# Kernel optimization log

Hardware: AMD Instinct MI355X
Metric: run time of the kernel (lower is better)

## Reference

```python
import jax, jax.numpy as jnp
import numpy as np

EMBED_DIM = 1024
NUM_HEADS = 16
SCALE = (EMBED_DIM // NUM_HEADS) ** -0.5  # 0.125


def setup_inputs() -> dict:
    key = jax.random.key(0)
    ks = jax.random.split(key, 9)
    B, S, E = 4, 2048, EMBED_DIM
    std = E ** -0.5
    x = jax.random.normal(ks[0], (B, S, E), dtype=jnp.float32)
    Wq = jax.random.normal(ks[1], (E, E), dtype=jnp.float32) * std
    bq = jax.random.normal(ks[2], (E,), dtype=jnp.float32) * 0.01
    Wk = jax.random.normal(ks[3], (E, E), dtype=jnp.float32) * std
    bk = jax.random.normal(ks[4], (E,), dtype=jnp.float32) * 0.01
    Wv = jax.random.normal(ks[5], (E, E), dtype=jnp.float32) * std
    bv = jax.random.normal(ks[6], (E,), dtype=jnp.float32) * 0.01
    Wo = jax.random.normal(ks[7], (E, E), dtype=jnp.float32) * std
    bo = jax.random.normal(ks[8], (E,), dtype=jnp.float32) * 0.01
    return {"x": x, "Wq": Wq, "bq": bq, "Wk": Wk, "bk": bk,
            "Wv": Wv, "bv": bv, "Wo": Wo, "bo": bo}


def reference(x, Wq, bq, Wk, bk, Wv, bv, Wo, bo):
    # torch nn.Linear: y = x @ W.T + b
    q = jnp.einsum('bse,fe->bsf', x, Wq) + bq   # [B,S,E]
    k = jnp.einsum('bse,fe->bsf', x, Wk) + bk
    v = jnp.einsum('bse,fe->bsf', x, Wv) + bv
    # Bilinear (no softmax) attention: scores = (Q K^T) * scale
    scores = jnp.einsum('bse,bte->bst', q, k) * SCALE  # [B,S,S]
    out = jnp.einsum('bst,bte->bse', scores, v)        # [B,S,E]
    return jnp.einsum('bse,fe->bsf', out, Wo) + bo
```

## Files before the change

### kernel.cpp

```cpp
#include <hip/hip_runtime.h>
#include <stdint.h>

typedef __bf16 bf16_t;
typedef __bf16 bf16x8 __attribute__((ext_vector_type(8)));
typedef __bf16 bf16x4 __attribute__((ext_vector_type(4)));
typedef float floatx4 __attribute__((ext_vector_type(4)));

__device__ __forceinline__ void async_copy16(const bf16_t* g, bf16_t* l) {
  __builtin_amdgcn_global_load_lds(
      (const __attribute__((address_space(1))) void*)g,
      (__attribute__((address_space(3))) void*)l, 16, 0, 0);
}

struct CvtSeg { const float* s; bf16_t* d; long n; };
struct CvtArgs { CvtSeg seg[5]; };

__global__ void cvt_multi(CvtArgs a) {
  CvtSeg sg = a.seg[blockIdx.y];
#pragma unroll
  for (int it = 0; it < 4; it++) {
    long i = (((long)blockIdx.x + (long)it * 2048) * 256 + threadIdx.x) * 4;
    if (i < sg.n) {
      float4 f = *(const float4*)(sg.s + i);
      bf16x4 o;
      o[0] = (bf16_t)f.x; o[1] = (bf16_t)f.y; o[2] = (bf16_t)f.z; o[3] = (bf16_t)f.w;
      *(bf16x4*)(sg.d + i) = o;
    }
  }
}

__global__ void cvt_mhalf(const bf16_t* __restrict__ mh, bf16_t* __restrict__ mt) {
  const long i = ((long)blockIdx.x * 256 + threadIdx.x) * 8;
  const long b = i >> 20;
  const long r = i & ((1L << 20) - 1);
  const bf16_t* h0 = mh + ((b * 2) << 20) + r;
  const bf16_t* h1 = h0 + (1L << 20);
  bf16x8 x0 = *(const bf16x8*)h0;
  bf16x8 x1 = *(const bf16x8*)h1;
  bf16x8 o;
#pragma unroll
  for (int j = 0; j < 8; j++) o[j] = (bf16_t)((float)x0[j] + (float)x1[j]);
  *(bf16x8*)(mt + i) = o;
}

__global__ __launch_bounds__(256, 2) void qkv3(
    const bf16_t* __restrict__ xb,
    const bf16_t* __restrict__ Wq, const bf16_t* __restrict__ Wk, const bf16_t* __restrict__ Wv,
    const float* __restrict__ bq, const float* __restrict__ bk, const float* __restrict__ bv,
    bf16_t* __restrict__ qout, bf16_t* __restrict__ kT, bf16_t* __restrict__ vT) {
  __shared__ bf16_t As[2 * 4096];
  __shared__ bf16_t Bsh[3][2 * 4096];
  const int L = blockIdx.x;
  const int V = (L & 7) * 64 + (L >> 3);
  const int batch = V >> 7;
  const int rr_   = V & 127;
  const int n0 = (rr_ & 7) * 128;
  const int m0 = (rr_ >> 3) * 128;

  const int tid = threadIdx.x, lane = tid & 63, w = tid >> 6;
  const int wr = w >> 1, wc = w & 1, quad = lane >> 4, lm = lane & 15;
  const int ar = lane >> 2;
  const int ak = (((lane & 3) ^ ((ar >> 1) & 3))) * 8;
  const int swz = (lm >> 1) & 3;

  const bf16_t* ag0 = xb + (long)batch * (2048L * 1024) + (long)(m0 + w * 16 + ar) * 1024 + ak;
  const bf16_t* ag1 = ag0 + 64L * 1024;
  const bf16_t* Wp[3] = {Wq, Wk, Wv};
  const bf16_t* bg0[3];
  const bf16_t* bg1[3];
#pragma unroll
  for (int p = 0; p < 3; p++) {
    bg0[p] = Wp[p] + (long)(n0 + w * 16 + ar) * 1024 + ak;
    bg1[p] = bg0[p] + 64L * 1024;
  }

  floatx4 acc[3][4][4];
#pragma unroll
  for (int p = 0; p < 3; p++)
#pragma unroll
    for (int r = 0; r < 4; r++)
#pragma unroll
      for (int c = 0; c < 4; c++)
        acc[p][r][c] = (floatx4){0.f, 0.f, 0.f, 0.f};

  {
    bf16_t* la = As + w * 512;
    async_copy16(ag0, la);
    async_copy16(ag1, la + 2048);
#pragma unroll
    for (int p = 0; p < 3; p++) {
      bf16_t* lb = Bsh[p] + w * 512;
      async_copy16(bg0[p], lb);
      async_copy16(bg1[p], lb + 2048);
    }
  }
  for (int i = 0; i < 32; i++) {
    __syncthreads();
    if (i + 1 < 32) {
      const int buf = (i + 1) & 1, k0 = (i + 1) * 32;
      bf16_t* la = As + buf * 4096 + w * 512;
      async_copy16(ag0 + k0, la);
      async_copy16(ag1 + k0, la + 2048);
#pragma unroll
      for (int p = 0; p < 3; p++) {
        bf16_t* lb = Bsh[p] + buf * 4096 + w * 512;
        async_copy16(bg0[p] + k0, lb);
        async_copy16(bg1[p] + k0, lb + 2048);
      }
    }
    const bf16_t* Ar = As + (i & 1) * 4096;
    bf16x8 afr[4];
#pragma unroll
    for (int r = 0; r < 4; r++)
      afr[r] = *(const bf16x8*)&Ar[(wr * 64 + r * 16 + lm) * 32 + (quad ^ swz) * 8];
#pragma unroll
    for (int p = 0; p < 3; p++) {
      const bf16_t* Br = Bsh[p] + (i & 1) * 4096;
      bf16x8 bfr[4];
#pragma unroll
      for (int c = 0; c < 4; c++)
        bfr[c] = *(const bf16x8*)&Br[(wc * 64 + c * 16 + lm) * 32 + (quad ^ swz) * 8];
#pragma unroll
      for (int r = 0; r < 4; r++)
#pragma unroll
        for (int c = 0; c < 4; c++)
          acc[p][r][c] = __builtin_amdgcn_mfma_f32_16x16x32_bf16(afr[r], bfr[c], acc[p][r][c], 0, 0, 0);
    }
  }

  const int rowBase = m0 + wr * 64, colBase = n0 + wc * 64;
  {
    bf16_t* C = qout + (long)batch * (2048L * 1024);
#pragma unroll
    for (int r = 0; r < 4; r++) {
      const int row = rowBase + r * 16 + quad * 4;
#pragma unroll
      for (int c = 0; c < 4; c++) {
        const int col = colBase + c * 16 + lm;
        const float bv_ = bq[col];
#pragma unroll
        for (int i = 0; i < 4; i++)
          C[(long)(row + i) * 1024 + col] = (bf16_t)(acc[0][r][c][i] + bv_);
      }
    }
  }
#pragma unroll
  for (int p = 1; p < 3; p++) {
    bf16_t* C = ((p == 1) ? kT : vT) + (long)batch * (1024L * 2048);
    const float* bias = (p == 1) ? bk : bv;
#pragma unroll
    for (int r = 0; r < 4; r++) {
      const int row = rowBase + r * 16 + quad * 4;
#pragma unroll
      for (int c = 0; c < 4; c++) {
        const int col = colBase + c * 16 + lm;
        const float bv_ = bias[col];
        bf16x4 pk;
#pragma unroll
        for (int i = 0; i < 4; i++) pk[i] = (bf16_t)(acc[p][r][c][i] + bv_);
        *(bf16x4*)(C + (long)col * 2048 + row) = pk;
      }
    }
  }
}

template<int OUT_MODE, bool HAS_BIAS, int TOTAL, int BPZ, int KSPLIT>
__global__ __launch_bounds__(256) void gemm_nt128(
    const bf16_t* __restrict__ A, const bf16_t* __restrict__ B,
    void* __restrict__ C, const float* __restrict__ bias,
    int lda, int ldb, int nk, long sA, long sB, long sC, int ldc, float alpha) {
  __shared__ bf16_t As[2 * 4096];
  __shared__ bf16_t Bs[2 * 4096];
  const int L = blockIdx.x;
  const int V = (L & 7) * (TOTAL / 8) + (L >> 3);
  const int zz = V / BPZ;
  const int r_ = V % BPZ;
  const int batch = zz / KSPLIT;
  const long koff = (long)(zz % KSPLIT) * ((long)nk * 32);
  const int n0 = (r_ & 7) * 128;
  const int m0 = (r_ >> 3) * 128;

  const int tid = threadIdx.x, lane = tid & 63, w = tid >> 6;
  const int wr = w >> 1, wc = w & 1, quad = lane >> 4, lm = lane & 15;
  const int ar = lane >> 2;
  const int ak = (((lane & 3) ^ ((ar >> 1) & 3))) * 8;
  const int swz = (lm >> 1) & 3;

  const bf16_t* Ab = A + (long)batch * sA + koff;
  const bf16_t* Bb = B + (long)batch * sB + koff;
  const bf16_t* ag0 = Ab + (long)(m0 + w * 16 + ar) * lda + ak;
  const bf16_t* ag1 = ag0 + (long)64 * lda;
  const bf16_t* bg0 = Bb + (long)(n0 + w * 16 + ar) * ldb + ak;
  const bf16_t* bg1 = bg0 + (long)64 * ldb;

  floatx4 acc[4][4];
#pragma unroll
  for (int r = 0; r < 4; r++)
#pragma unroll
    for (int c = 0; c < 4; c++) acc[r][c] = (floatx4){0.f, 0.f, 0.f, 0.f};

  {
    async_copy16(ag0, As + w * 512);
    async_copy16(ag1, As + w * 512 + 2048);
    async_copy16(bg0, Bs + w * 512);
    async_copy16(bg1, Bs + w * 512 + 2048);
  }
  for (int i = 0; i < nk; i++) {
    __syncthreads();
    if (i + 1 < nk) {
      const int buf = (i + 1) & 1, k0 = (i + 1) * 32;
      async_copy16(ag0 + k0, As + buf * 4096 + w * 512);
      async_copy16(ag1 + k0, As + buf * 4096 + w * 512 + 2048);
      async_copy16(bg0 + k0, Bs + buf * 4096 + w * 512);
      async_copy16(bg1 + k0, Bs + buf * 4096 + w * 512 + 2048);
    }
    const bf16_t* Ar = As + (i & 1) * 4096;
    const bf16_t* Br = Bs + (i & 1) * 4096;
    bf16x8 afr[4], bfr[4];
#pragma unroll
    for (int r = 0; r < 4; r++)
      afr[r] = *(const bf16x8*)&Ar[(wr * 64 + r * 16 + lm) * 32 + (quad ^ swz) * 8];
#pragma unroll
    for (int c = 0; c < 4; c++)
      bfr[c] = *(const bf16x8*)&Br[(wc * 64 + c * 16 + lm) * 32 + (quad ^ swz) * 8];
#pragma unroll
    for (int r = 0; r < 4; r++)
#pragma unroll
      for (int c = 0; c < 4; c++)
        acc[r][c] = __builtin_amdgcn_mfma_f32_16x16x32_bf16(afr[r], bfr[c], acc[r][c], 0, 0, 0);
  }

  const int rowBase = m0 + wr * 64, colBase = n0 + wc * 64;
  if (OUT_MODE == 0) {
    bf16_t* Cb = (bf16_t*)C + (long)zz * sC;
#pragma unroll
    for (int r = 0; r < 4; r++) {
      const int row = rowBase + r * 16 + quad * 4;
#pragma unroll
      for (int c = 0; c < 4; c++) {
        const int col = colBase + c * 16 + lm;
        const float bv_ = HAS_BIAS ? bias[col] : 0.f;
#pragma unroll
        for (int i = 0; i < 4; i++)
          Cb[(long)(row + i) * ldc + col] = (bf16_t)(acc[r][c][i] * alpha + bv_);
      }
    }
  } else {
    float* Cf = (float*)C + (long)zz * sC;
#pragma unroll
    for (int r = 0; r < 4; r++) {
      const int row = rowBase + r * 16 + quad * 4;
#pragma unroll
      for (int c = 0; c < 4; c++) {
        const int col = colBase + c * 16 + lm;
        const float bv_ = HAS_BIAS ? bias[col] : 0.f;
#pragma unroll
        for (int i = 0; i < 4; i++)
          Cf[(long)(row + i) * ldc + col] = acc[r][c][i] * alpha + bv_;
      }
    }
  }
}

extern "C" void kernel_launch(void* const* d_in, const int* in_sizes, int n_in,
                              void* d_out, int out_size, void* d_ws, size_t ws_size,
                              hipStream_t stream) {
  const float* x  = (const float*)d_in[0];
  const float* Wq = (const float*)d_in[1];
  const float* bq = (const float*)d_in[2];
  const float* Wk = (const float*)d_in[3];
  const float* bk = (const float*)d_in[4];
  const float* Wv = (const float*)d_in[5];
  const float* bv = (const float*)d_in[6];
  const float* Wo = (const float*)d_in[7];
  const float* bo = (const float*)d_in[8];
  float* out = (float*)d_out;

  const long NX = 8192L * 1024;
  const long NW = 1024L * 1024;

  bf16_t* ws  = (bf16_t*)d_ws;
  bf16_t* xb  = ws;
  bf16_t* Wqb = xb + NX;
  bf16_t* Wkb = Wqb + NW;
  bf16_t* Wvb = Wkb + NW;
  bf16_t* Wob = Wvb + NW;
  bf16_t* qb  = Wob + NW;
  bf16_t* kT  = qb + NX;
  bf16_t* vT  = kT + NX;
  bf16_t* Mh  = xb;
  bf16_t* Mtb = kT;
  bf16_t* Pb  = vT;

  CvtArgs ca;
  ca.seg[0] = {x,  xb,  NX};
  ca.seg[1] = {Wq, Wqb, NW};
  ca.seg[2] = {Wk, Wkb, NW};
  ca.seg[3] = {Wv, Wvb, NW};
  ca.seg[4] = {Wo, Wob, NW};
  cvt_multi<<<dim3(2048, 5), 256, 0, stream>>>(ca);

  qkv3<<<dim3(512), 256, 0, stream>>>(xb, Wqb, Wkb, Wvb, bq, bk, bv, qb, kT, vT);

  gemm_nt128<0, false, 512, 64, 2><<<dim3(512), 256, 0, stream>>>(
      vT, kT, Mh, nullptr, 2048, 2048, 32,
      1024L * 2048, 1024L * 2048, 1024L * 1024, 1024, 0.125f);

  cvt_mhalf<<<dim3(2048), 256, 0, stream>>>(Mh, Mtb);

  gemm_nt128<0, false, 512, 128, 1><<<dim3(512), 256, 0, stream>>>(
      qb, Mtb, Pb, nullptr, 1024, 1024, 32,
      2048L * 1024, 1024L * 1024, 2048L * 1024, 1024, 1.0f);

  gemm_nt128<2, true, 512, 128, 1><<<dim3(512), 256, 0, stream>>>(
      Pb, Wob, out, bo, 1024, 1024, 32,
      2048L * 1024, 0L, 2048L * 1024, 1024, 1.0f);
}
```

Before: 239.5 us.

## Fold Wo into per-batch KV matrix and deepen GEMM pipeline to 4 stages

Reassociates the output projection: first computes per-batch G = Wo·(KᵀV)ᵀ, a 1024x1024 GEMM per batch, then out = Q·Gᵀ + bo. This removes one of the two large 2048x1024x1024 GEMMs per batch and replaces it with a smaller 1024³ one. The operand order of the KᵀV GEMM is swapped to suit the new orientation. Separately, the GEMM kernel now uses a 4-buffer LDS ring with two tiles in flight and explicit vmcnt waits instead of double buffering. This doubles shared memory use, which may reduce occupancy.

After: 232.4 us. -3.0%, faster.

```diff
diff --git a/kernel.cpp b/kernel.cpp
--- a/kernel.cpp
+++ b/kernel.cpp
@@ -169,8 +169,8 @@
     const bf16_t* __restrict__ A, const bf16_t* __restrict__ B,
     void* __restrict__ C, const float* __restrict__ bias,
     int lda, int ldb, int nk, long sA, long sB, long sC, int ldc, float alpha) {
-  __shared__ bf16_t As[2 * 4096];
-  __shared__ bf16_t Bs[2 * 4096];
+  __shared__ bf16_t As[4 * 4096];
+  __shared__ bf16_t Bs[4 * 4096];
   const int L = blockIdx.x;
   const int V = (L & 7) * (TOTAL / 8) + (L >> 3);
   const int zz = V / BPZ;
@@ -193,29 +193,35 @@
   const bf16_t* bg0 = Bb + (long)(n0 + w * 16 + ar) * ldb + ak;
   const bf16_t* bg1 = bg0 + (long)64 * ldb;
 
+  auto STAGE = [&](int t, int buf) {
+    const int k0 = t * 32;
+    async_copy16(ag0 + k0, As + buf * 4096 + w * 512);
+    async_copy16(ag1 + k0, As + buf * 4096 + w * 512 + 2048);
+    async_copy16(bg0 + k0, Bs + buf * 4096 + w * 512);
+    async_copy16(bg1 + k0, Bs + buf * 4096 + w * 512 + 2048);
+  };
+
   floatx4 acc[4][4];
 #pragma unroll
   for (int r = 0; r < 4; r++)
 #pragma unroll
     for (int c = 0; c < 4; c++) acc[r][c] = (floatx4){0.f, 0.f, 0.f, 0.f};
 
-  {
-    async_copy16(ag0, As + w * 512);
-    async_copy16(ag1, As + w * 512 + 2048);
-    async_copy16(bg0, Bs + w * 512);
-    async_copy16(bg1, Bs + w * 512 + 2048);
-  }
+  STAGE(0, 0);
+  STAGE(1, 1);
   for (int i = 0; i < nk; i++) {
-    __syncthreads();
-    if (i + 1 < nk) {
-      const int buf = (i + 1) & 1, k0 = (i + 1) * 32;
-      async_copy16(ag0 + k0, As + buf * 4096 + w * 512);
-      async_copy16(ag1 + k0, As + buf * 4096 + w * 512 + 2048);
-      async_copy16(bg0 + k0, Bs + buf * 4096 + w * 512);
-      async_copy16(bg1 + k0, Bs + buf * 4096 + w * 512 + 2048);
-    }
-    const bf16_t* Ar = As + (i & 1) * 4096;
-    const bf16_t* Br = Bs + (i & 1) * 4096;
+    if (i + 2 < nk) {
+      STAGE(i + 2, (i + 2) & 3);
+      asm volatile("s_waitcnt vmcnt(8)" ::: "memory");
+    } else if (i + 1 < nk) {
+      asm volatile("s_waitcnt vmcnt(4)" ::: "memory");
+    } else {
+      asm volatile("s_waitcnt vmcnt(0)" ::: "memory");
+    }
+    __builtin_amdgcn_s_barrier();
+    asm volatile("" ::: "memory");
+    const bf16_t* Ar = As + (i & 3) * 4096;
+    const bf16_t* Br = Bs + (i & 3) * 4096;
     bf16x8 afr[4], bfr[4];
 #pragma unroll
     for (int r = 0; r < 4; r++)
@@ -288,9 +294,9 @@
   bf16_t* qb  = Wob + NW;
   bf16_t* kT  = qb + NX;
   bf16_t* vT  = kT + NX;
-  bf16_t* Mh  = xb;
-  bf16_t* Mtb = kT;
-  bf16_t* Pb  = vT;
+  bf16_t* Mh   = xb;
+  bf16_t* MtTb = kT;
+  bf16_t* Gb   = vT;
 
   CvtArgs ca;
   ca.seg[0] = {x,  xb,  NX};
@@ -303,16 +309,16 @@
   qkv3<<<dim3(512), 256, 0, stream>>>(xb, Wqb, Wkb, Wvb, bq, bk, bv, qb, kT, vT);
 
   gemm_nt128<0, false, 512, 64, 2><<<dim3(512), 256, 0, stream>>>(
-      vT, kT, Mh, nullptr, 2048, 2048, 32,
+      kT, vT, Mh, nullptr, 2048, 2048, 32,
       1024L * 2048, 1024L * 2048, 1024L * 1024, 1024, 0.125f);
 
-  cvt_mhalf<<<dim3(2048), 256, 0, stream>>>(Mh, Mtb);
-
-  gemm_nt128<0, false, 512, 128, 1><<<dim3(512), 256, 0, stream>>>(
-      qb, Mtb, Pb, nullptr, 1024, 1024, 32,
+  cvt_mhalf<<<dim3(2048), 256, 0, stream>>>(Mh, MtTb);
+
+  gemm_nt128<0, false, 256, 64, 1><<<dim3(256), 256, 0, stream>>>(
+      Wob, MtTb, Gb, nullptr, 1024, 1024, 32,
+      0L, 1024L * 1024, 1024L * 1024, 1024, 1.0f);
+
+  gemm_nt128<2, true, 512, 128, 1><<<dim3(512), 256, 0, stream>>>(
+      qb, Gb, out, bo, 1024, 1024, 32,
       2048L * 1024, 1024L * 1024, 2048L * 1024, 1024, 1.0f);
-
-  gemm_nt128<2, true, 512, 128, 1><<<dim3(512), 256, 0, stream>>>(
-      Pb, Wob, out, bo, 1024, 1024, 32,
-      2048L * 1024, 0L, 2048L * 1024, 1024, 1.0f);
-}
+}
```

## Use 256x128 tiles with 8 waves per block for all GEMMs

Applied to the files above, without the earlier changes.

Doubles the M tile of the QKV and generic GEMM kernels to 256 rows and runs 512 threads (8 waves) per block, so each block loads each B tile once for twice as many output rows. The grid is halved to 256 blocks and the block-index remapping is adjusted. This cuts redundant B-operand traffic and the number of blocks, but uses more LDS per block and leaves fewer blocks than the 256 CUs might want for latency hiding. The unshown epilogue must also handle the 8-wave row layout, since wr now spans 0..3.

Measured after the change: 266.3 us. 1.11x slower.

```diff
diff --git a/kernel.cpp b/kernel.cpp
--- a/kernel.cpp
+++ b/kernel.cpp
@@ -43,19 +43,19 @@
   *(bf16x8*)(mt + i) = o;
 }
 
-__global__ __launch_bounds__(256, 2) void qkv3(
+__global__ __launch_bounds__(512, 2) void qkv3(
     const bf16_t* __restrict__ xb,
     const bf16_t* __restrict__ Wq, const bf16_t* __restrict__ Wk, const bf16_t* __restrict__ Wv,
     const float* __restrict__ bq, const float* __restrict__ bk, const float* __restrict__ bv,
     bf16_t* __restrict__ qout, bf16_t* __restrict__ kT, bf16_t* __restrict__ vT) {
-  __shared__ bf16_t As[2 * 4096];
+  __shared__ bf16_t As[2 * 8192];
   __shared__ bf16_t Bsh[3][2 * 4096];
   const int L = blockIdx.x;
-  const int V = (L & 7) * 64 + (L >> 3);
-  const int batch = V >> 7;
-  const int rr_   = V & 127;
+  const int V = (L & 7) * 32 + (L >> 3);
+  const int batch = V >> 6;
+  const int rr_   = V & 63;
   const int n0 = (rr_ & 7) * 128;
-  const int m0 = (rr_ >> 3) * 128;
+  const int m0 = (rr_ >> 3) * 256;
 
   const int tid = threadIdx.x, lane = tid & 63, w = tid >> 6;
   const int wr = w >> 1, wc = w & 1, quad = lane >> 4, lm = lane & 15;
@@ -63,16 +63,13 @@
   const int ak = (((lane & 3) ^ ((ar >> 1) & 3))) * 8;
   const int swz = (lm >> 1) & 3;
 
-  const bf16_t* ag0 = xb + (long)batch * (2048L * 1024) + (long)(m0 + w * 16 + ar) * 1024 + ak;
-  const bf16_t* ag1 = ag0 + 64L * 1024;
+  const bf16_t* ag0 = xb + (long)batch * (2048L * 1024) + (long)(m0 + w * 32 + ar) * 1024 + ak;
+  const bf16_t* ag1 = ag0 + 16L * 1024;
   const bf16_t* Wp[3] = {Wq, Wk, Wv};
   const bf16_t* bg0[3];
-  const bf16_t* bg1[3];
-#pragma unroll
-  for (int p = 0; p < 3; p++) {
+#pragma unroll
+  for (int p = 0; p < 3; p++)
     bg0[p] = Wp[p] + (long)(n0 + w * 16 + ar) * 1024 + ak;
-    bg1[p] = bg0[p] + 64L * 1024;
-  }
 
   floatx4 acc[3][4][4];
 #pragma unroll
@@ -84,31 +81,23 @@
         acc[p][r][c] = (floatx4){0.f, 0.f, 0.f, 0.f};
 
   {
-    bf16_t* la = As + w * 512;
-    async_copy16(ag0, la);
-    async_copy16(ag1, la + 2048);
-#pragma unroll
-    for (int p = 0; p < 3; p++) {
-      bf16_t* lb = Bsh[p] + w * 512;
-      async_copy16(bg0[p], lb);
-      async_copy16(bg1[p], lb + 2048);
-    }
+    async_copy16(ag0, As + w * 1024);
+    async_copy16(ag1, As + w * 1024 + 512);
+#pragma unroll
+    for (int p = 0; p < 3; p++)
+      async_copy16(bg0[p], Bsh[p] + w * 512);
   }
   for (int i = 0; i < 32; i++) {
     __syncthreads();
     if (i + 1 < 32) {
       const int buf = (i + 1) & 1, k0 = (i + 1) * 32;
-      bf16_t* la = As + buf * 4096 + w * 512;
-      async_copy16(ag0 + k0, la);
-      async_copy16(ag1 + k0, la + 2048);
-#pragma unroll
-      for (int p = 0; p < 3; p++) {
-        bf16_t* lb = Bsh[p] + buf * 4096 + w * 512;
-        async_copy16(bg0[p] + k0, lb);
-        async_copy16(bg1[p] + k0, lb + 2048);
-      }
-    }
-    const bf16_t* Ar = As + (i & 1) * 4096;
+      async_copy16(ag0 + k0, As + buf * 8192 + w * 1024);
+      async_copy16(ag1 + k0, As + buf * 8192 + w * 1024 + 512);
+#pragma unroll
+      for (int p = 0; p < 3; p++)
+        async_copy16(bg0[p] + k0, Bsh[p] + buf * 4096 + w * 512);
+    }
+    const bf16_t* Ar = As + (i & 1) * 8192;
     bf16x8 afr[4];
 #pragma unroll
     for (int r = 0; r < 4; r++)
@@ -165,11 +154,11 @@
 }
 
 template<int OUT_MODE, bool HAS_BIAS, int TOTAL, int BPZ, int KSPLIT>
-__global__ __launch_bounds__(256) void gemm_nt128(
+__global__ __launch_bounds__(512, 2) void gemm_w8(
     const bf16_t* __restrict__ A, const bf16_t* __restrict__ B,
     void* __restrict__ C, const float* __restrict__ bias,
     int lda, int ldb, int nk, long sA, long sB, long sC, int ldc, float alpha) {
-  __shared__ bf16_t As[2 * 4096];
+  __shared__ bf16_t As[2 * 8192];
   __shared__ bf16_t Bs[2 * 4096];
   const int L = blockIdx.x;
   const int V = (L & 7) * (TOTAL / 8) + (L >> 3);
@@ -178,7 +167,7 @@
   const int batch = zz / KSPLIT;
   const long koff = (long)(zz % KSPLIT) * ((long)nk * 32);
   const int n0 = (r_ & 7) * 128;
-  const int m0 = (r_ >> 3) * 128;
+  const int m0 = (r_ >> 3) * 256;
 
   const int tid = threadIdx.x, lane = tid & 63, w = tid >> 6;
   const int wr = w >> 1, wc = w & 1, quad = lane >> 4, lm = lane & 15;
@@ -188,10 +177,9 @@
 
   const bf16_t* Ab = A + (long)batch * sA + koff;
   const bf16_t* Bb = B + (long)batch * sB + koff;
-  const bf16_t* ag0 = Ab + (long)(m0 + w * 16 + ar) * lda + ak;
-  const bf16_t* ag1 = ag0 + (long)64 * lda;
+  const bf16_t* ag0 = Ab + (long)(m0 + w * 32 + ar) * lda + ak;
+  const bf16_t* ag1 = ag0 + (long)16 * lda;
   const bf16_t* bg0 = Bb + (long)(n0 + w * 16 + ar) * ldb + ak;
-  const bf16_t* bg1 = bg0 + (long)64 * ldb;
 
   floatx4 acc[4][4];
 #pragma unroll
@@ -200,21 +188,19 @@
     for (int c = 0; c < 4; c++) acc[r][c] = (floatx4){0.f, 0.f, 0.f, 0.f};
 
   {
-    async_copy16(ag0, As + w * 512);
-    async_copy16(ag1, As + w * 512 + 2048);
+    async_copy16(ag0, As + w * 1024);
+    async_copy16(ag1, As + w * 1024 + 512);
     async_copy16(bg0, Bs + w * 512);
-    async_copy16(bg1, Bs + w * 512 + 2048);
   }
   for (int i = 0; i < nk; i++) {
     __syncthreads();
     if (i + 1 < nk) {
       const int buf = (i + 1) & 1, k0 = (i + 1) * 32;
-      async_copy16(ag0 + k0, As + buf * 4096 + w * 512);
-      async_copy16(ag1 + k0, As + buf * 4096 + w * 512 + 2048);
+      async_copy16(ag0 + k0, As + buf * 8192 + w * 1024);
+      async_copy16(ag1 + k0, As + buf * 8192 + w * 1024 + 512);
       async_copy16(bg0 + k0, Bs + buf * 4096 + w * 512);
-      async_copy16(bg1 + k0, Bs + buf * 4096 + w * 512 + 2048);
-    }
-    const bf16_t* Ar = As + (i & 1) * 4096;
+    }
+    const bf16_t* Ar = As + (i & 1) * 8192;
     const bf16_t* Br = Bs + (i & 1) * 4096;
     bf16x8 afr[4], bfr[4];
 #pragma unroll
@@ -300,19 +286,19 @@
   ca.seg[4] = {Wo, Wob, NW};
   cvt_multi<<<dim3(2048, 5), 256, 0, stream>>>(ca);
 
-  qkv3<<<dim3(512), 256, 0, stream>>>(xb, Wqb, Wkb, Wvb, bq, bk, bv, qb, kT, vT);
-
-  gemm_nt128<0, false, 512, 64, 2><<<dim3(512), 256, 0, stream>>>(
+  qkv3<<<dim3(256), 512, 0, stream>>>(xb, Wqb, Wkb, Wvb, bq, bk, bv, qb, kT, vT);
+
+  gemm_w8<0, false, 256, 32, 2><<<dim3(256), 512, 0, stream>>>(
       vT, kT, Mh, nullptr, 2048, 2048, 32,
       1024L * 2048, 1024L * 2048, 1024L * 1024, 1024, 0.125f);
 
   cvt_mhalf<<<dim3(2048), 256, 0, stream>>>(Mh, Mtb);
 
-  gemm_nt128<0, false, 512, 128, 1><<<dim3(512), 256, 0, stream>>>(
+  gemm_w8<0, false, 256, 64, 1><<<dim3(256), 512, 0, stream>>>(
       qb, Mtb, Pb, nullptr, 1024, 1024, 32,
       2048L * 1024, 1024L * 1024, 2048L * 1024, 1024, 1.0f);
 
-  gemm_nt128<2, true, 512, 128, 1><<<dim3(512), 256, 0, stream>>>(
+  gemm_w8<2, true, 256, 64, 1><<<dim3(256), 512, 0, stream>>>(
       Pb, Wob, out, bo, 1024, 1024, 32,
       2048L * 1024, 0L, 2048L * 1024, 1024, 1.0f);
 }
```

## Deepen split-K for middle GEMMs and use output buffer as partial-sum scratch

Applied to the files above, without the earlier changes.

The K^T·V-style GEMM now splits K four ways and the Q·M GEMM two ways. Each launches 1024 blocks instead of 512 to fill more CUs, and GEMM launch bounds allow 4 blocks per SU. Partial results go to the free xb region and to the output buffer used as scratch, then separate elementwise kernels (msum4, psum2) reduce them. This trades extra partial-sum memory traffic and two reduction launches for better occupancy and parallelism on the 1024-deep reductions.

New measurement: 250.5 us. +4.6%, slower.

```diff
diff --git a/kernel.cpp b/kernel.cpp
--- a/kernel.cpp
+++ b/kernel.cpp
@@ -29,18 +29,29 @@
   }
 }
 
-__global__ void cvt_mhalf(const bf16_t* __restrict__ mh, bf16_t* __restrict__ mt) {
+__global__ void msum4(const bf16_t* __restrict__ s0, const bf16_t* __restrict__ s1,
+                      bf16_t* __restrict__ d) {
   const long i = ((long)blockIdx.x * 256 + threadIdx.x) * 8;
-  const long b = i >> 20;
-  const long r = i & ((1L << 20) - 1);
-  const bf16_t* h0 = mh + ((b * 2) << 20) + r;
-  const bf16_t* h1 = h0 + (1L << 20);
-  bf16x8 x0 = *(const bf16x8*)h0;
-  bf16x8 x1 = *(const bf16x8*)h1;
+  bf16x8 a = *(const bf16x8*)(s0 + i);
+  bf16x8 b = *(const bf16x8*)(s0 + i + 4194304);
+  bf16x8 c = *(const bf16x8*)(s1 + i);
+  bf16x8 e = *(const bf16x8*)(s1 + i + 4194304);
   bf16x8 o;
 #pragma unroll
-  for (int j = 0; j < 8; j++) o[j] = (bf16_t)((float)x0[j] + (float)x1[j]);
-  *(bf16x8*)(mt + i) = o;
+  for (int j = 0; j < 8; j++)
+    o[j] = (bf16_t)((float)a[j] + (float)b[j] + (float)c[j] + (float)e[j]);
+  *(bf16x8*)(d + i) = o;
+}
+
+__global__ void psum2(const bf16_t* __restrict__ s0, const bf16_t* __restrict__ s1,
+                      bf16_t* __restrict__ d) {
+  const long i = ((long)blockIdx.x * 256 + threadIdx.x) * 8;
+  bf16x8 a = *(const bf16x8*)(s0 + i);
+  bf16x8 b = *(const bf16x8*)(s1 + i);
+  bf16x8 o;
+#pragma unroll
+  for (int j = 0; j < 8; j++) o[j] = (bf16_t)((float)a[j] + (float)b[j]);
+  *(bf16x8*)(d + i) = o;
 }
 
 __global__ __launch_bounds__(256, 2) void qkv3(
@@ -165,10 +176,10 @@
 }
 
 template<int OUT_MODE, bool HAS_BIAS, int TOTAL, int BPZ, int KSPLIT>
-__global__ __launch_bounds__(256) void gemm_nt128(
+__global__ __launch_bounds__(256, 4) void gemm_ks(
     const bf16_t* __restrict__ A, const bf16_t* __restrict__ B,
-    void* __restrict__ C, const float* __restrict__ bias,
-    int lda, int ldb, int nk, long sA, long sB, long sC, int ldc, float alpha) {
+    void* __restrict__ C0, void* __restrict__ C1, const float* __restrict__ bias,
+    int lda, int ldb, int nk, long sA, long sB, long pS, long sC, int ldc, float alpha) {
   __shared__ bf16_t As[2 * 4096];
   __shared__ bf16_t Bs[2 * 4096];
   const int L = blockIdx.x;
@@ -176,7 +187,8 @@
   const int zz = V / BPZ;
   const int r_ = V % BPZ;
   const int batch = zz / KSPLIT;
-  const long koff = (long)(zz % KSPLIT) * ((long)nk * 32);
+  const int kp = zz % KSPLIT;
+  const long koff = (long)kp * ((long)nk * 32);
   const int n0 = (r_ & 7) * 128;
   const int m0 = (r_ >> 3) * 128;
 
@@ -232,7 +244,13 @@
 
   const int rowBase = m0 + wr * 64, colBase = n0 + wc * 64;
   if (OUT_MODE == 0) {
-    bf16_t* Cb = (bf16_t*)C + (long)zz * sC;
+    bf16_t* Cp;
+    if (KSPLIT == 1) {
+      Cp = (bf16_t*)C0 + (long)batch * sC;
+    } else {
+      bf16_t* base = (bf16_t*)((kp < KSPLIT / 2) ? C0 : C1);
+      Cp = base + (long)(kp % (KSPLIT / 2)) * pS + (long)batch * sC;
+    }
 #pragma unroll
     for (int r = 0; r < 4; r++) {
       const int row = rowBase + r * 16 + quad * 4;
@@ -242,11 +260,11 @@
         const float bv_ = HAS_BIAS ? bias[col] : 0.f;
 #pragma unroll
         for (int i = 0; i < 4; i++)
-          Cb[(long)(row + i) * ldc + col] = (bf16_t)(acc[r][c][i] * alpha + bv_);
+          Cp[(long)(row + i) * ldc + col] = (bf16_t)(acc[r][c][i] * alpha + bv_);
       }
     }
   } else {
-    float* Cf = (float*)C + (long)zz * sC;
+    float* Cp = (float*)C0 + (long)batch * sC;
 #pragma unroll
     for (int r = 0; r < 4; r++) {
       const int row = rowBase + r * 16 + quad * 4;
@@ -256,7 +274,7 @@
         const float bv_ = HAS_BIAS ? bias[col] : 0.f;
 #pragma unroll
         for (int i = 0; i < 4; i++)
-          Cf[(long)(row + i) * ldc + col] = acc[r][c][i] * alpha + bv_;
+          Cp[(long)(row + i) * ldc + col] = acc[r][c][i] * alpha + bv_;
       }
     }
   }
@@ -288,7 +306,7 @@
   bf16_t* qb  = Wob + NW;
   bf16_t* kT  = qb + NX;
   bf16_t* vT  = kT + NX;
-  bf16_t* Mh  = xb;
+  bf16_t* outb = (bf16_t*)out;
   bf16_t* Mtb = kT;
   bf16_t* Pb  = vT;
 
@@ -302,17 +320,19 @@
 
   qkv3<<<dim3(512), 256, 0, stream>>>(xb, Wqb, Wkb, Wvb, bq, bk, bv, qb, kT, vT);
 
-  gemm_nt128<0, false, 512, 64, 2><<<dim3(512), 256, 0, stream>>>(
-      vT, kT, Mh, nullptr, 2048, 2048, 32,
-      1024L * 2048, 1024L * 2048, 1024L * 1024, 1024, 0.125f);
-
-  cvt_mhalf<<<dim3(2048), 256, 0, stream>>>(Mh, Mtb);
-
-  gemm_nt128<0, false, 512, 128, 1><<<dim3(512), 256, 0, stream>>>(
-      qb, Mtb, Pb, nullptr, 1024, 1024, 32,
-      2048L * 1024, 1024L * 1024, 2048L * 1024, 1024, 1.0f);
-
-  gemm_nt128<2, true, 512, 128, 1><<<dim3(512), 256, 0, stream>>>(
-      Pb, Wob, out, bo, 1024, 1024, 32,
-      2048L * 1024, 0L, 2048L * 1024, 1024, 1.0f);
-}
+  gemm_ks<0, false, 1024, 64, 4><<<dim3(1024), 256, 0, stream>>>(
+      vT, kT, xb, outb, nullptr, 2048, 2048, 16,
+      1024L * 2048, 1024L * 2048, 4194304L, 1024L * 1024, 1024, 0.125f);
+
+  msum4<<<dim3(2048), 256, 0, stream>>>(xb, outb, Mtb);
+
+  gemm_ks<0, false, 1024, 128, 2><<<dim3(1024), 256, 0, stream>>>(
+      qb, Mtb, xb, outb, nullptr, 1024, 1024, 16,
+      2048L * 1024, 1024L * 1024, 0L, 2048L * 1024, 1024, 1.0f);
+
+  psum2<<<dim3(4096), 256, 0, stream>>>(xb, outb, Pb);
+
+  gemm_ks<2, true, 512, 128, 1><<<dim3(512), 256, 0, stream>>>(
+      Pb, Wob, out, nullptr, bo, 1024, 1024, 32,
+      2048L * 1024, 0L, 0L, 2048L * 1024, 1024, 1.0f);
+}
```
